# Kernel tuning notes

Measured on AMD Instinct MI355X. Metric: run time of the kernel, lower is better.

Reference implementation:

```python
import jax, jax.numpy as jnp
import numpy as np
import math

C = 256
HEADS = 8
WS1 = (8, 8)
SS1 = (0, 0)
WS2 = (8, 8)
SS2 = (4, 4)
CPB_HIDDEN = 512


def _rel_pos_index(ws):
    coords = np.stack(np.meshgrid(np.arange(ws[0]), np.arange(ws[1]), indexing="ij")).reshape(2, -1)
    rel = (coords[:, :, None] - coords[:, None, :]).transpose(1, 2, 0).astype(np.int64)
    rel[..., 0] += ws[0] - 1
    rel[..., 1] += ws[1] - 1
    rel[..., 0] *= 2 * ws[1] - 1
    return rel.sum(-1).reshape(-1)


def _coords_table(ws):
    ch = np.arange(-(ws[0] - 1), ws[0], dtype=np.float32)
    cw = np.arange(-(ws[1] - 1), ws[1], dtype=np.float32)
    t = np.stack(np.meshgrid(ch, cw, indexing="ij"), axis=-1)
    t[..., 0] /= ws[0] - 1
    t[..., 1] /= ws[1] - 1
    t *= 8.0
    t = np.sign(t) * np.log2(np.abs(t) + 1.0) / 3.0
    return t.reshape(-1, 2)


def _swin_mask(pH, pW, ws, ss):
    # standard swin shifted-window attention mask, [num_windows, N, N]
    m = np.zeros((pH, pW), dtype=np.float32)
    cnt = 0.0
    hs = ((0, pH - ws[0]), (pH - ws[0], pH - ss[0]), (pH - ss[0], pH))
    wl = ((0, pW - ws[1]), (pW - ws[1], pW - ss[1]), (pW - ss[1], pW))
    for h0, h1 in hs:
        for w0, w1 in wl:
            m[h0:h1, w0:w1] = cnt
            cnt += 1.0
    m = m.reshape(pH // ws[0], ws[0], pW // ws[1], ws[1]).transpose(0, 2, 1, 3).reshape(-1, ws[0] * ws[1])
    diff = m[:, None, :] - m[:, :, None]
    return np.where(diff != 0.0, -100.0, 0.0).astype(np.float32)


def _swin_attn_v2(x, qkv_w, qkv_b, proj_w, proj_b, logit_scale, cpb_w1, cpb_b1, cpb_w2, ws, ss, num_heads):
    # torchvision ShiftedWindowAttentionV2 forward (dropout=0, eval)
    B, H, W, Cc = x.shape
    L = qkv_b.shape[0] // 3
    qkv_b = jnp.concatenate([qkv_b[:L], jnp.zeros_like(qkv_b[L:2 * L]), qkv_b[2 * L:]])  # v2 zeroes key bias
    pad_b = (ws[0] - H % ws[0]) % ws[0]
    pad_r = (ws[1] - W % ws[1]) % ws[1]
    x = jnp.pad(x, ((0, 0), (0, pad_b), (0, pad_r), (0, 0)))
    pH, pW = H + pad_b, W + pad_r
    s0 = 0 if ws[0] >= pH else ss[0]
    s1 = 0 if ws[1] >= pW else ss[1]
    shifted = (s0 > 0) or (s1 > 0)
    if shifted:
        x = jnp.roll(x, (-s0, -s1), axis=(1, 2))
    nH, nW = pH // ws[0], pW // ws[1]
    N = ws[0] * ws[1]
    xw = x.reshape(B, nH, ws[0], nW, ws[1], Cc).transpose(0, 1, 3, 2, 4, 5).reshape(B * nH * nW, N, Cc)
    qkv = (xw @ qkv_w.T + qkv_b).reshape(-1, N, 3, num_heads, Cc // num_heads).transpose(2, 0, 3, 1, 4)
    q, k, v = qkv[0], qkv[1], qkv[2]
    qn = q / jnp.maximum(jnp.linalg.norm(q, axis=-1, keepdims=True), 1e-12)
    kn = k / jnp.maximum(jnp.linalg.norm(k, axis=-1, keepdims=True), 1e-12)
    scale = jnp.exp(jnp.minimum(logit_scale, math.log(100.0)))  # [heads,1,1]
    attn = jnp.einsum("bhnd,bhmd->bhnm", qn, kn) * scale[None]
    # continuous relative position bias (v2)
    table = jnp.asarray(_coords_table(ws))
    bias_table = jax.nn.relu(table @ cpb_w1.T + cpb_b1) @ cpb_w2.T
    rpb = bias_table[_rel_pos_index(ws)].reshape(N, N, num_heads).transpose(2, 0, 1)
    attn = attn + 16.0 * jax.nn.sigmoid(rpb)[None]
    if shifted:
        mask = jnp.asarray(_swin_mask(pH, pW, ws, (s0, s1)))  # [nWin, N, N]
        attn = (attn.reshape(B, nH * nW, num_heads, N, N) + mask[None, :, None]).reshape(-1, num_heads, N, N)
    attn = jax.nn.softmax(attn, axis=-1)
    out = jnp.einsum("bhnm,bhmd->bhnd", attn, v).transpose(0, 2, 1, 3).reshape(-1, N, Cc)
    out = out @ proj_w.T + proj_b
    out = out.reshape(B, nH, nW, ws[0], ws[1], Cc).transpose(0, 1, 3, 2, 4, 5).reshape(B, pH, pW, Cc)
    if shifted:
        out = jnp.roll(out, (s0, s1), axis=(1, 2))
    return out[:, :H, :W, :]


def _make_params(keys):
    return {
        "qkv_w": jax.random.normal(keys[0], (3 * C, C), dtype=jnp.float32) * 0.02,
        "qkv_b": jax.random.normal(keys[1], (3 * C,), dtype=jnp.float32) * 0.02,
        "proj_w": jax.random.normal(keys[2], (C, C), dtype=jnp.float32) * 0.02,
        "proj_b": jax.random.normal(keys[3], (C,), dtype=jnp.float32) * 0.02,
        "logit_scale": jnp.full((HEADS, 1, 1), math.log(10.0), dtype=jnp.float32),
        "cpb_w1": jax.random.normal(keys[4], (CPB_HIDDEN, 2), dtype=jnp.float32) * 0.02,
        "cpb_b1": jnp.zeros((CPB_HIDDEN,), dtype=jnp.float32),
        "cpb_w2": jax.random.normal(keys[5], (HEADS, CPB_HIDDEN), dtype=jnp.float32) * 0.02,
    }


def setup_inputs() -> dict:
    key = jax.random.key(0)
    ks = jax.random.split(key, 13)
    d = {"src": jax.random.normal(ks[0], (4, 8, C, 64, 64), dtype=jnp.float32)}
    for pre, off in (("a1", 1), ("a2", 7)):
        for name, val in _make_params(ks[off:off + 6]).items():
            d[pre + "_" + name] = val
    return d


def reference(src, a1_qkv_w, a1_qkv_b, a1_proj_w, a1_proj_b, a1_logit_scale, a1_cpb_w1, a1_cpb_b1, a1_cpb_w2, a2_qkv_w, a2_qkv_b, a2_proj_w, a2_proj_b, a2_logit_scale, a2_cpb_w1, a2_cpb_b1, a2_cpb_w2):
    B, T, Cc, H, W = src.shape
    x = src.reshape(B * T, Cc, H, W).transpose(0, 2, 3, 1)  # [BT,H,W,C]
    x = x + _swin_attn_v2(x, a1_qkv_w, a1_qkv_b, a1_proj_w, a1_proj_b, a1_logit_scale, a1_cpb_w1, a1_cpb_b1, a1_cpb_w2, WS1, SS1, HEADS)
    x = x + _swin_attn_v2(x, a2_qkv_w, a2_qkv_b, a2_proj_w, a2_proj_b, a2_logit_scale, a2_cpb_w1, a2_cpb_b1, a2_cpb_w2, WS2, SS2, HEADS)
    return x.transpose(0, 3, 1, 2).reshape(src.shape)
```

## Files before the change

kernel.cpp:

```cpp
#include <hip/hip_runtime.h>


typedef short bf16x8 __attribute__((ext_vector_type(8)));
typedef float f32x4 __attribute__((ext_vector_type(4)));

__device__ __forceinline__ unsigned short f2bf(float f) {
    union { float f; unsigned int u; } v; v.f = f;
    return (unsigned short)((v.u + 0x7fffu + ((v.u >> 16) & 1u)) >> 16);
}
__device__ __forceinline__ float bf2f(unsigned short b) {
    union { unsigned int u; float f; } v; v.u = ((unsigned int)b) << 16;
    return v.f;
}
__device__ __forceinline__ f32x4 mfma_bf16(bf16x8 a, bf16x8 b, f32x4 c) {
    return __builtin_amdgcn_mfma_f32_16x16x32_bf16(a, b, c, 0, 0, 0);
}

__device__ __forceinline__ int region_of(int wh, int ww, int t) {
    int th = t >> 3, tw = t & 7;
    int rh = (wh == 7) ? ((th < 4) ? 1 : 2) : 0;
    int rw = (ww == 7) ? ((tw < 4) ? 1 : 2) : 0;
    return rh * 3 + rw;
}

__global__ __launch_bounds__(256) void k_setup(
    const float* __restrict__ qkvw1, const float* __restrict__ projw1,
    const float* __restrict__ qkvw2, const float* __restrict__ projw2,
    const float* __restrict__ w1a, const float* __restrict__ b1a, const float* __restrict__ w2a,
    const float* __restrict__ w1b, const float* __restrict__ b1b, const float* __restrict__ w2b,
    unsigned short* __restrict__ qw1, unsigned short* __restrict__ pw1,
    unsigned short* __restrict__ qw2, unsigned short* __restrict__ pw2,
    float* __restrict__ bt1, float* __restrict__ bt2)
{
    int b = blockIdx.x, t = threadIdx.x;
    if (b < 512) {
        int idx = b * 256 + t;
        #pragma unroll
        for (int r = 0; r < 4; r++) {
            int i = idx + r * 131072;
            if (i < 196608)        qw1[i]          = f2bf(qkvw1[i]);
            else if (i < 262144)   pw1[i - 196608] = f2bf(projw1[i - 196608]);
            else if (i < 458752)   qw2[i - 262144] = f2bf(qkvw2[i - 262144]);
            else                   pw2[i - 458752] = f2bf(projw2[i - 458752]);
        }
    } else {
        int a = b - 512;
        const float* w1 = a ? w1b : w1a;
        const float* b1 = a ? b1b : b1a;
        const float* w2 = a ? w2b : w2a;
        float* out = a ? bt2 : bt1;
        int k = t;
        if (k >= 225) return;
        int ih = k / 15, iw = k % 15;
        float v0 = (float)(ih - 7) / 7.0f * 8.0f;
        float v1 = (float)(iw - 7) / 7.0f * 8.0f;
        float t0 = (v0 >= 0.f ? 1.f : -1.f) * log2f(fabsf(v0) + 1.f) / 3.0f;
        float t1 = (v1 >= 0.f ? 1.f : -1.f) * log2f(fabsf(v1) + 1.f) / 3.0f;
        float acc[8] = {0.f, 0.f, 0.f, 0.f, 0.f, 0.f, 0.f, 0.f};
        for (int c = 0; c < 512; c++) {
            float hc = t0 * w1[2 * c] + t1 * w1[2 * c + 1] + b1[c];
            hc = fmaxf(hc, 0.f);
            #pragma unroll
            for (int h = 0; h < 8; h++) acc[h] += hc * w2[h * 512 + c];
        }
        #pragma unroll
        for (int h = 0; h < 8; h++) out[k * 8 + h] = 16.f / (1.f + expf(-acc[h]));
    }
}

__global__ __launch_bounds__(256) void t_in(const float* __restrict__ src, float* __restrict__ dst) {
    __shared__ float tile[32][33];
    int img = blockIdx.z, hw0 = blockIdx.x * 32, c0 = blockIdx.y * 32;
    int x = threadIdx.x & 31, y = threadIdx.x >> 5;
    #pragma unroll
    for (int k = 0; k < 4; k++)
        tile[y + k * 8][x] = src[((size_t)img * 256 + c0 + y + k * 8) * 4096 + hw0 + x];
    __syncthreads();
    #pragma unroll
    for (int k = 0; k < 4; k++)
        dst[((size_t)img * 4096 + hw0 + y + k * 8) * 256 + c0 + x] = tile[x][y + k * 8];
}

__global__ __launch_bounds__(256) void t_out(const float* __restrict__ src, float* __restrict__ dst) {
    __shared__ float tile[32][33];
    int img = blockIdx.z, hw0 = blockIdx.x * 32, c0 = blockIdx.y * 32;
    int x = threadIdx.x & 31, y = threadIdx.x >> 5;
    #pragma unroll
    for (int k = 0; k < 4; k++)
        tile[y + k * 8][x] = src[((size_t)img * 4096 + hw0 + y + k * 8) * 256 + c0 + x];
    __syncthreads();
    #pragma unroll
    for (int k = 0; k < 4; k++)
        dst[((size_t)img * 256 + c0 + y + k * 8) * 4096 + hw0 + x] = tile[x][y + k * 8];
}

__global__ __launch_bounds__(256, 2) void k_swin(
    const float* __restrict__ Xin,
    const unsigned short* __restrict__ Wq,
    const float* __restrict__ bq,
    const float* __restrict__ lsc,
    const float* __restrict__ btab,
    const unsigned short* __restrict__ Wp,
    const float* __restrict__ bp,
    unsigned short* __restrict__ AO,
    float* __restrict__ Xout,
    int shift, int masked)
{
    __shared__ __align__(16) unsigned short sX[64 * 264];
    __shared__ __align__(16) unsigned short sQKV[64 * 200];
    __shared__ __align__(16) unsigned short sP[64 * 72];
    __shared__ __align__(16) unsigned short sVt[64 * 72];
    __shared__ float sInv[4 * 64];

    const int tid = threadIdx.x;
    const int wv = tid >> 6, lane = tid & 63, quad = lane >> 4, nn = lane & 15;
    const int win = blockIdx.x;
    const int bt = win >> 6, wh = (win >> 3) & 7, ww = win & 7;
    const f32x4 zero4 = {0.f, 0.f, 0.f, 0.f};

    {
        int tok = tid >> 2, part = tid & 3;
        int h = (wh * 8 + (tok >> 3) + shift) & 63;
        int w = (ww * 8 + (tok & 7) + shift) & 63;
        const float* srcp = Xin + ((size_t)(bt * 4096 + h * 64 + w)) * 256 + part * 64;
        unsigned short* dstp = sX + tok * 264 + part * 64;
        #pragma unroll
        for (int c = 0; c < 64; c += 4) {
            float4 v = *(const float4*)(srcp + c);
            unsigned int p0 = (unsigned int)f2bf(v.x) | ((unsigned int)f2bf(v.y) << 16);
            unsigned int p1 = (unsigned int)f2bf(v.z) | ((unsigned int)f2bf(v.w) << 16);
            uint2 o; o.x = p0; o.y = p1;
            *(uint2*)(dstp + c) = o;
        }
    }
    __syncthreads();

    for (int p = 0; p < 4; p++) {
        f32x4 acc[4][3];
        #pragma unroll
        for (int rt = 0; rt < 4; rt++)
            #pragma unroll
            for (int c = 0; c < 3; c++) acc[rt][c] = zero4;

        int wrow[3], cbase[3], kindv[3];
        #pragma unroll
        for (int c = 0; c < 3; c++) {
            int ct = wv * 3 + c;
            int sec = ct >> 1;
            int kind = sec >> 1;
            int head = 2 * p + (sec & 1);
            wrow[c] = kind * 256 + head * 32 + (ct & 1) * 16 + nn;
            cbase[c] = ct * 16 + nn;
            kindv[c] = kind;
        }
        #pragma unroll
        for (int ks = 0; ks < 8; ks++) {
            bf16x8 a[4], b[3];
            #pragma unroll
            for (int rt = 0; rt < 4; rt++)
                a[rt] = *(const bf16x8*)(sX + (rt * 16 + nn) * 264 + ks * 32 + quad * 8);
            #pragma unroll
            for (int c = 0; c < 3; c++)
                b[c] = *(const bf16x8*)(Wq + (size_t)wrow[c] * 256 + ks * 32 + quad * 8);
            #pragma unroll
            for (int rt = 0; rt < 4; rt++)
                #pragma unroll
                for (int c = 0; c < 3; c++)
                    acc[rt][c] = mfma_bf16(a[rt], b[c], acc[rt][c]);
        }
        #pragma unroll
        for (int c = 0; c < 3; c++) {
            float bias = (kindv[c] == 1) ? 0.f : bq[wrow[c]];
            #pragma unroll
            for (int rt = 0; rt < 4; rt++)
                #pragma unroll
                for (int r = 0; r < 4; r++) {
                    int tokr = rt * 16 + quad * 4 + r;
                    sQKV[tokr * 200 + cbase[c]] = f2bf(acc[rt][c][r] + bias);
                }
        }
        __syncthreads();

        {
            int t = tid & 63, which = tid >> 6;
            const unsigned short* row = sQKV + t * 200 + which * 32;
            float ss = 0.f;
            #pragma unroll
            for (int cc = 0; cc < 32; cc++) { float v = bf2f(row[cc]); ss += v * v; }
            sInv[which * 64 + t] = 1.f / fmaxf(sqrtf(ss), 1e-12f);
            #pragma unroll
            for (int dd = 0; dd < 16; dd++) {
                int d = which * 16 + dd;
                sVt[d * 72 + t] = sQKV[t * 200 + 128 + d];
            }
        }
        __syncthreads();

        for (int hh = 0; hh < 2; hh++) {
            const int head = 2 * p + hh;
            const float scale = __expf(fminf(lsc[head], 4.605170185988092f));

            bf16x8 aq = *(const bf16x8*)(sQKV + (wv * 16 + nn) * 200 + hh * 32 + quad * 8);
            f32x4 S[4];
            #pragma unroll
            for (int ct = 0; ct < 4; ct++) {
                bf16x8 bk = *(const bf16x8*)(sQKV + (ct * 16 + nn) * 200 + 64 + hh * 32 + quad * 8);
                S[ct] = mfma_bf16(aq, bk, zero4);
            }

            const float* invq = sInv + hh * 64;
            const float* invk = sInv + (2 + hh) * 64;
            const int i_base = wv * 16 + quad * 4;
            float rowm[4] = {-3.0e38f, -3.0e38f, -3.0e38f, -3.0e38f};
            int ri[4];
            #pragma unroll
            for (int r = 0; r < 4; r++) ri[r] = masked ? region_of(wh, ww, i_base + r) : 0;

            #pragma unroll
            for (int ct = 0; ct < 4; ct++) {
                int j = ct * 16 + nn;
                float ivk = invk[j];
                int rj = masked ? region_of(wh, ww, j) : 0;
                #pragma unroll
                for (int r = 0; r < 4; r++) {
                    int i = i_base + r;
                    float v = S[ct][r] * invq[i] * ivk * scale;
                    int rel = ((i >> 3) - (j >> 3) + 7) * 15 + ((i & 7) - (j & 7) + 7);
                    v += btab[rel * 8 + head];
                    if (masked && (ri[r] != rj)) v += -100.f;
                    S[ct][r] = v;
                    rowm[r] = fmaxf(rowm[r], v);
                }
            }
            #pragma unroll
            for (int r = 0; r < 4; r++) {
                float m = rowm[r];
                m = fmaxf(m, __shfl_xor(m, 1));
                m = fmaxf(m, __shfl_xor(m, 2));
                m = fmaxf(m, __shfl_xor(m, 4));
                m = fmaxf(m, __shfl_xor(m, 8));
                rowm[r] = m;
            }
            float rsum[4] = {0.f, 0.f, 0.f, 0.f};
            #pragma unroll
            for (int ct = 0; ct < 4; ct++)
                #pragma unroll
                for (int r = 0; r < 4; r++) {
                    float e = __expf(S[ct][r] - rowm[r]);
                    S[ct][r] = e;
                    rsum[r] += e;
                }
            #pragma unroll
            for (int r = 0; r < 4; r++) {
                float s = rsum[r];
                s += __shfl_xor(s, 1);
                s += __shfl_xor(s, 2);
                s += __shfl_xor(s, 4);
                s += __shfl_xor(s, 8);
                rsum[r] = 1.f / s;
            }
            #pragma unroll
            for (int ct = 0; ct < 4; ct++)
                #pragma unroll
                for (int r = 0; r < 4; r++)
                    sP[(i_base + r) * 72 + ct * 16 + nn] = f2bf(S[ct][r] * rsum[r]);

            bf16x8 ap0 = *(const bf16x8*)(sP + (wv * 16 + nn) * 72 + quad * 8);
            bf16x8 ap1 = *(const bf16x8*)(sP + (wv * 16 + nn) * 72 + 32 + quad * 8);
            #pragma unroll
            for (int ct2 = 0; ct2 < 2; ct2++) {
                bf16x8 bv0 = *(const bf16x8*)(sVt + (hh * 32 + ct2 * 16 + nn) * 72 + quad * 8);
                bf16x8 bv1 = *(const bf16x8*)(sVt + (hh * 32 + ct2 * 16 + nn) * 72 + 32 + quad * 8);
                f32x4 O = mfma_bf16(ap0, bv0, zero4);
                O = mfma_bf16(ap1, bv1, O);
                #pragma unroll
                for (int r = 0; r < 4; r++) {
                    int tokr = i_base + r;
                    AO[((size_t)win * 64 + tokr) * 256 + head * 32 + ct2 * 16 + nn] = f2bf(O[r]);
                }
            }
        }
        __syncthreads();
    }

    {
        int tok = tid >> 2, part = tid & 3;
        const unsigned short* srcp = AO + ((size_t)win * 64 + tok) * 256 + part * 64;
        unsigned short* dstp = sX + tok * 264 + part * 64;
        #pragma unroll
        for (int c = 0; c < 64; c += 8)
            *(uint4*)(dstp + c) = *(const uint4*)(srcp + c);
    }
    __syncthreads();

    f32x4 pacc[4][4];
    #pragma unroll
    for (int rt = 0; rt < 4; rt++)
        #pragma unroll
        for (int c = 0; c < 4; c++) pacc[rt][c] = zero4;

    int prow[4];
    #pragma unroll
    for (int c = 0; c < 4; c++) prow[c] = (wv * 4 + c) * 16 + nn;

    #pragma unroll
    for (int ks = 0; ks < 8; ks++) {
        bf16x8 a[4], b[4];
        #pragma unroll
        for (int rt = 0; rt < 4; rt++)
            a[rt] = *(const bf16x8*)(sX + (rt * 16 + nn) * 264 + ks * 32 + quad * 8);
        #pragma unroll
        for (int c = 0; c < 4; c++)
            b[c] = *(const bf16x8*)(Wp + (size_t)prow[c] * 256 + ks * 32 + quad * 8);
        #pragma unroll
        for (int rt = 0; rt < 4; rt++)
            #pragma unroll
            for (int c = 0; c < 4; c++)
                pacc[rt][c] = mfma_bf16(a[rt], b[c], pacc[rt][c]);
    }

    #pragma unroll
    for (int c = 0; c < 4; c++) {
        int chan = prow[c];
        float bias = bp[chan];
        #pragma unroll
        for (int rt = 0; rt < 4; rt++)
            #pragma unroll
            for (int r = 0; r < 4; r++) {
                int tok = rt * 16 + quad * 4 + r;
                int h = (wh * 8 + (tok >> 3) + shift) & 63;
                int w = (ww * 8 + (tok & 7) + shift) & 63;
                size_t idx = ((size_t)(bt * 4096 + h * 64 + w)) * 256 + chan;
                Xout[idx] = pacc[rt][c][r] + bias + Xin[idx];
            }
    }
}

extern "C" void kernel_launch(void* const* d_in, const int* in_sizes, int n_in,
                              void* d_out, int out_size, void* d_ws, size_t ws_size,
                              hipStream_t stream) {
    (void)in_sizes; (void)n_in; (void)out_size; (void)ws_size;

    const float* src        = (const float*)d_in[0];
    const float* a1_qkv_w   = (const float*)d_in[1];
    const float* a1_qkv_b   = (const float*)d_in[2];
    const float* a1_proj_w  = (const float*)d_in[3];
    const float* a1_proj_b  = (const float*)d_in[4];
    const float* a1_ls      = (const float*)d_in[5];
    const float* a1_w1      = (const float*)d_in[6];
    const float* a1_b1      = (const float*)d_in[7];
    const float* a1_w2      = (const float*)d_in[8];
    const float* a2_qkv_w   = (const float*)d_in[9];
    const float* a2_qkv_b   = (const float*)d_in[10];
    const float* a2_proj_w  = (const float*)d_in[11];
    const float* a2_proj_b  = (const float*)d_in[12];
    const float* a2_ls      = (const float*)d_in[13];
    const float* a2_w1      = (const float*)d_in[14];
    const float* a2_b1      = (const float*)d_in[15];
    const float* a2_w2      = (const float*)d_in[16];

    char* ws = (char*)d_ws;
    const size_t SZ_X = 134217728;
    float* X0 = (float*)(ws);
    float* X1 = (float*)(ws + SZ_X);
    unsigned short* AO  = (unsigned short*)(ws + 2 * SZ_X);
    unsigned short* qw1 = (unsigned short*)(ws + 2 * SZ_X + 67108864);
    unsigned short* qw2 = qw1 + 196608;
    unsigned short* pw1 = qw2 + 196608;
    unsigned short* pw2 = pw1 + 65536;
    float* bt1 = (float*)(pw2 + 65536);
    float* bt2 = bt1 + 1800;

    k_setup<<<514, 256, 0, stream>>>(a1_qkv_w, a1_proj_w, a2_qkv_w, a2_proj_w,
                                     a1_w1, a1_b1, a1_w2, a2_w1, a2_b1, a2_w2,
                                     qw1, pw1, qw2, pw2, bt1, bt2);
    t_in<<<dim3(128, 8, 32), 256, 0, stream>>>(src, X0);

    k_swin<<<2048, 256, 0, stream>>>(X0, qw1, a1_qkv_b, a1_ls, bt1, pw1, a1_proj_b, AO, X1, 0, 0);
    k_swin<<<2048, 256, 0, stream>>>(X1, qw2, a2_qkv_b, a2_ls, bt2, pw2, a2_proj_b, AO, X0, 4, 1);

    t_out<<<dim3(128, 8, 32), 256, 0, stream>>>(X0, (float*)d_out);
}
```

Measured before the change: 927.8 us.

## Fuse QK norms and V transpose into QKV epilogue, vectorize transposes

The QKV GEMM's column ownership is remapped so each wave holds whole q/k head rows. Their L2 norms are computed in registers with shuffles, and V is written directly transposed into sVt. This drops a sync and the separate norm/transpose pass, and shrinks sQKV. The relative-position bias table is staged in shared memory, and per-thread bias offsets and mask adds are precomputed once per block. The transpose kernels now use float4 loads and stores over 128-wide tiles, and the input load uses 16-byte stores. The norm is now computed from fp32 values rather than bf16-rounded ones, and the larger shared-memory use may affect occupancy.

```diff
diff --git a/kernel.cpp b/kernel.cpp
--- a/kernel.cpp
+++ b/kernel.cpp
@@ -69,29 +69,48 @@
 }
 
 __global__ __launch_bounds__(256) void t_in(const float* __restrict__ src, float* __restrict__ dst) {
-    __shared__ float tile[32][33];
-    int img = blockIdx.z, hw0 = blockIdx.x * 32, c0 = blockIdx.y * 32;
-    int x = threadIdx.x & 31, y = threadIdx.x >> 5;
-    #pragma unroll
-    for (int k = 0; k < 4; k++)
-        tile[y + k * 8][x] = src[((size_t)img * 256 + c0 + y + k * 8) * 4096 + hw0 + x];
+    __shared__ float tile[32][132];
+    int img = blockIdx.z, hw0 = blockIdx.x * 128, c0 = blockIdx.y * 32;
+    int tid = threadIdx.x;
+    #pragma unroll
+    for (int k = 0; k < 4; k++) {
+        int cl = (tid >> 5) + k * 8;
+        int hw4 = (tid & 31) * 4;
+        float4 v = *(const float4*)(src + ((size_t)img * 256 + c0 + cl) * 4096 + hw0 + hw4);
+        *(float4*)&tile[cl][hw4] = v;
+    }
     __syncthreads();
     #pragma unroll
-    for (int k = 0; k < 4; k++)
-        dst[((size_t)img * 4096 + hw0 + y + k * 8) * 256 + c0 + x] = tile[x][y + k * 8];
+    for (int j = 0; j < 4; j++) {
+        int hwl = (tid >> 3) + j * 32;
+        int c4 = (tid & 7) * 4;
+        float4 o;
+        o.x = tile[c4 + 0][hwl]; o.y = tile[c4 + 1][hwl];
+        o.z = tile[c4 + 2][hwl]; o.w = tile[c4 + 3][hwl];
+        *(float4*)(dst + ((size_t)img * 4096 + hw0 + hwl) * 256 + c0 + c4) = o;
+    }
 }
 
 __global__ __launch_bounds__(256) void t_out(const float* __restrict__ src, float* __restrict__ dst) {
-    __shared__ float tile[32][33];
-    int img = blockIdx.z, hw0 = blockIdx.x * 32, c0 = blockIdx.y * 32;
-    int x = threadIdx.x & 31, y = threadIdx.x >> 5;
-    #pragma unroll
-    for (int k = 0; k < 4; k++)
-        tile[y + k * 8][x] = src[((size_t)img * 4096 + hw0 + y + k * 8) * 256 + c0 + x];
+    __shared__ float tile[32][132];
+    int img = blockIdx.z, hw0 = blockIdx.x * 128, c0 = blockIdx.y * 32;
+    int tid = threadIdx.x;
+    #pragma unroll
+    for (int j = 0; j < 4; j++) {
+        int hwl = (tid >> 3) + j * 32;
+        int c4 = (tid & 7) * 4;
+        float4 v = *(const float4*)(src + ((size_t)img * 4096 + hw0 + hwl) * 256 + c0 + c4);
+        tile[c4 + 0][hwl] = v.x; tile[c4 + 1][hwl] = v.y;
+        tile[c4 + 2][hwl] = v.z; tile[c4 + 3][hwl] = v.w;
+    }
     __syncthreads();
     #pragma unroll
-    for (int k = 0; k < 4; k++)
-        dst[((size_t)img * 256 + c0 + y + k * 8) * 4096 + hw0 + x] = tile[x][y + k * 8];
+    for (int k = 0; k < 4; k++) {
+        int cl = (tid >> 5) + k * 8;
+        int hw4 = (tid & 31) * 4;
+        float4 o = *(const float4*)&tile[cl][hw4];
+        *(float4*)(dst + ((size_t)img * 256 + c0 + cl) * 4096 + hw0 + hw4) = o;
+    }
 }
 
 __global__ __launch_bounds__(256, 2) void k_swin(
@@ -107,16 +126,22 @@
     int shift, int masked)
 {
     __shared__ __align__(16) unsigned short sX[64 * 264];
-    __shared__ __align__(16) unsigned short sQKV[64 * 200];
+    __shared__ __align__(16) unsigned short sQKV[64 * 136];
     __shared__ __align__(16) unsigned short sP[64 * 72];
     __shared__ __align__(16) unsigned short sVt[64 * 72];
     __shared__ float sInv[4 * 64];
+    __shared__ float sBias[8 * 225];
 
     const int tid = threadIdx.x;
     const int wv = tid >> 6, lane = tid & 63, quad = lane >> 4, nn = lane & 15;
     const int win = blockIdx.x;
     const int bt = win >> 6, wh = (win >> 3) & 7, ww = win & 7;
     const f32x4 zero4 = {0.f, 0.f, 0.f, 0.f};
+
+    for (int i = tid; i < 1800; i += 256) {
+        int h = i / 225, rel = i - h * 225;
+        sBias[i] = btab[rel * 8 + h];
+    }
 
     {
         int tok = tid >> 2, part = tid & 3;
@@ -125,15 +150,36 @@
         const float* srcp = Xin + ((size_t)(bt * 4096 + h * 64 + w)) * 256 + part * 64;
         unsigned short* dstp = sX + tok * 264 + part * 64;
         #pragma unroll
-        for (int c = 0; c < 64; c += 4) {
-            float4 v = *(const float4*)(srcp + c);
-            unsigned int p0 = (unsigned int)f2bf(v.x) | ((unsigned int)f2bf(v.y) << 16);
-            unsigned int p1 = (unsigned int)f2bf(v.z) | ((unsigned int)f2bf(v.w) << 16);
-            uint2 o; o.x = p0; o.y = p1;
-            *(uint2*)(dstp + c) = o;
+        for (int c = 0; c < 64; c += 8) {
+            float4 v0 = *(const float4*)(srcp + c);
+            float4 v1 = *(const float4*)(srcp + c + 4);
+            uint4 o;
+            o.x = (unsigned int)f2bf(v0.x) | ((unsigned int)f2bf(v0.y) << 16);
+            o.y = (unsigned int)f2bf(v0.z) | ((unsigned int)f2bf(v0.w) << 16);
+            o.z = (unsigned int)f2bf(v1.x) | ((unsigned int)f2bf(v1.y) << 16);
+            o.w = (unsigned int)f2bf(v1.z) | ((unsigned int)f2bf(v1.w) << 16);
+            *(uint4*)(dstp + c) = o;
         }
     }
     __syncthreads();
+
+    int reloff[4][4];
+    float madd[4][4];
+    #pragma unroll
+    for (int ct = 0; ct < 4; ct++) {
+        int j = ct * 16 + nn;
+        int rj = region_of(wh, ww, j);
+        #pragma unroll
+        for (int r = 0; r < 4; r++) {
+            int i = wv * 16 + quad * 4 + r;
+            reloff[ct][r] = ((i >> 3) - (j >> 3) + 7) * 15 + ((i & 7) - (j & 7) + 7);
+            madd[ct][r] = (masked && (region_of(wh, ww, i) != rj)) ? -100.f : 0.f;
+        }
+    }
+
+    const int kind = wv >> 1;
+    const int hsel = wv & 1;
+    const int vc = wv * 16 + nn;
 
     for (int p = 0; p < 4; p++) {
         f32x4 acc[4][3];
@@ -142,17 +188,11 @@
             #pragma unroll
             for (int c = 0; c < 3; c++) acc[rt][c] = zero4;
 
-        int wrow[3], cbase[3], kindv[3];
-        #pragma unroll
-        for (int c = 0; c < 3; c++) {
-            int ct = wv * 3 + c;
-            int sec = ct >> 1;
-            int kind = sec >> 1;
-            int head = 2 * p + (sec & 1);
-            wrow[c] = kind * 256 + head * 32 + (ct & 1) * 16 + nn;
-            cbase[c] = ct * 16 + nn;
-            kindv[c] = kind;
-        }
+        int wrow[3];
+        wrow[0] = kind * 256 + (2 * p + hsel) * 32 + nn;
+        wrow[1] = wrow[0] + 16;
+        wrow[2] = 512 + (2 * p + (vc >> 5)) * 32 + (vc & 31);
+
         #pragma unroll
         for (int ks = 0; ks < 8; ks++) {
             bf16x8 a[4], b[3];
@@ -168,66 +208,79 @@
                 for (int c = 0; c < 3; c++)
                     acc[rt][c] = mfma_bf16(a[rt], b[c], acc[rt][c]);
         }
-        #pragma unroll
-        for (int c = 0; c < 3; c++) {
-            float bias = (kindv[c] == 1) ? 0.f : bq[wrow[c]];
+
+        float ssq[4][4];
+        #pragma unroll
+        for (int rt = 0; rt < 4; rt++)
+            #pragma unroll
+            for (int r = 0; r < 4; r++) ssq[rt][r] = 0.f;
+
+        #pragma unroll
+        for (int ctl = 0; ctl < 2; ctl++) {
+            float bias = kind ? 0.f : bq[wrow[ctl]];
+            int col = wv * 32 + ctl * 16 + nn;
             #pragma unroll
             for (int rt = 0; rt < 4; rt++)
                 #pragma unroll
                 for (int r = 0; r < 4; r++) {
-                    int tokr = rt * 16 + quad * 4 + r;
-                    sQKV[tokr * 200 + cbase[c]] = f2bf(acc[rt][c][r] + bias);
+                    float val = acc[rt][ctl][r] + bias;
+                    ssq[rt][r] += val * val;
+                    sQKV[(rt * 16 + quad * 4 + r) * 136 + col] = f2bf(val);
                 }
         }
+        {
+            float bv = bq[wrow[2]];
+            #pragma unroll
+            for (int rt = 0; rt < 4; rt++) {
+                ushort4 pk;
+                pk.x = f2bf(acc[rt][2][0] + bv);
+                pk.y = f2bf(acc[rt][2][1] + bv);
+                pk.z = f2bf(acc[rt][2][2] + bv);
+                pk.w = f2bf(acc[rt][2][3] + bv);
+                *(ushort4*)(sVt + vc * 72 + rt * 16 + quad * 4) = pk;
+            }
+        }
+        #pragma unroll
+        for (int rt = 0; rt < 4; rt++)
+            #pragma unroll
+            for (int r = 0; r < 4; r++) {
+                float s = ssq[rt][r];
+                s += __shfl_xor(s, 1);
+                s += __shfl_xor(s, 2);
+                s += __shfl_xor(s, 4);
+                s += __shfl_xor(s, 8);
+                if (nn == 0)
+                    sInv[wv * 64 + rt * 16 + quad * 4 + r] = 1.f / fmaxf(sqrtf(s), 1e-12f);
+            }
         __syncthreads();
 
-        {
-            int t = tid & 63, which = tid >> 6;
-            const unsigned short* row = sQKV + t * 200 + which * 32;
-            float ss = 0.f;
-            #pragma unroll
-            for (int cc = 0; cc < 32; cc++) { float v = bf2f(row[cc]); ss += v * v; }
-            sInv[which * 64 + t] = 1.f / fmaxf(sqrtf(ss), 1e-12f);
-            #pragma unroll
-            for (int dd = 0; dd < 16; dd++) {
-                int d = which * 16 + dd;
-                sVt[d * 72 + t] = sQKV[t * 200 + 128 + d];
-            }
-        }
-        __syncthreads();
-
+        #pragma unroll
         for (int hh = 0; hh < 2; hh++) {
             const int head = 2 * p + hh;
             const float scale = __expf(fminf(lsc[head], 4.605170185988092f));
-
-            bf16x8 aq = *(const bf16x8*)(sQKV + (wv * 16 + nn) * 200 + hh * 32 + quad * 8);
+            const float* bh = sBias + head * 225;
+
+            bf16x8 aq = *(const bf16x8*)(sQKV + (wv * 16 + nn) * 136 + hh * 32 + quad * 8);
             f32x4 S[4];
             #pragma unroll
             for (int ct = 0; ct < 4; ct++) {
-                bf16x8 bk = *(const bf16x8*)(sQKV + (ct * 16 + nn) * 200 + 64 + hh * 32 + quad * 8);
+                bf16x8 bk = *(const bf16x8*)(sQKV + (ct * 16 + nn) * 136 + 64 + hh * 32 + quad * 8);
                 S[ct] = mfma_bf16(aq, bk, zero4);
             }
 
-            const float* invq = sInv + hh * 64;
-            const float* invk = sInv + (2 + hh) * 64;
             const int i_base = wv * 16 + quad * 4;
+            float iq[4];
+            #pragma unroll
+            for (int r = 0; r < 4; r++) iq[r] = sInv[hh * 64 + i_base + r];
+
             float rowm[4] = {-3.0e38f, -3.0e38f, -3.0e38f, -3.0e38f};
-            int ri[4];
-            #pragma unroll
-            for (int r = 0; r < 4; r++) ri[r] = masked ? region_of(wh, ww, i_base + r) : 0;
-
             #pragma unroll
             for (int ct = 0; ct < 4; ct++) {
                 int j = ct * 16 + nn;
-                float ivk = invk[j];
-                int rj = masked ? region_of(wh, ww, j) : 0;
+                float ivk = sInv[(2 + hh) * 64 + j];
                 #pragma unroll
                 for (int r = 0; r < 4; r++) {
-                    int i = i_base + r;
-                    float v = S[ct][r] * invq[i] * ivk * scale;
-                    int rel = ((i >> 3) - (j >> 3) + 7) * 15 + ((i & 7) - (j & 7) + 7);
-                    v += btab[rel * 8 + head];
-                    if (masked && (ri[r] != rj)) v += -100.f;
+                    float v = S[ct][r] * iq[r] * ivk * scale + bh[reloff[ct][r]] + madd[ct][r];
                     S[ct][r] = v;
                     rowm[r] = fmaxf(rowm[r], v);
                 }
@@ -374,10 +427,10 @@
     k_setup<<<514, 256, 0, stream>>>(a1_qkv_w, a1_proj_w, a2_qkv_w, a2_proj_w,
                                      a1_w1, a1_b1, a1_w2, a2_w1, a2_b1, a2_w2,
                                      qw1, pw1, qw2, pw2, bt1, bt2);
-    t_in<<<dim3(128, 8, 32), 256, 0, stream>>>(src, X0);
+    t_in<<<dim3(32, 8, 32), 256, 0, stream>>>(src, X0);
 
     k_swin<<<2048, 256, 0, stream>>>(X0, qw1, a1_qkv_b, a1_ls, bt1, pw1, a1_proj_b, AO, X1, 0, 0);
     k_swin<<<2048, 256, 0, stream>>>(X1, qw2, a2_qkv_b, a2_ls, bt2, pw2, a2_proj_b, AO, X0, 4, 1);
 
-    t_out<<<dim3(128, 8, 32), 256, 0, stream>>>(X0, (float*)d_out);
-}
+    t_out<<<dim3(32, 8, 32), 256, 0, stream>>>(X0, (float*)d_out);
+}
```

Result: slower. 978.8 us (+5.5%).
